# Performance work log

Hardware: AMD Instinct MI355X
Metric: run time of the kernel (lower is better)

## Reference

```python
import jax, jax.numpy as jnp
import numpy as np

N = 50000
E = 800000
IN_C, HID, OUT_C, HEADS = 128, 64, 32, 2
NEG_SLOPE = 0.2


def _add_self_loops(edge_index, n):
    loop = jnp.arange(n, dtype=edge_index.dtype)
    return jnp.concatenate([edge_index, jnp.stack([loop, loop])], axis=1)


def gcn_conv(x, edge_index, W, b, n):
    ei = _add_self_loops(edge_index, n)
    src, dst = ei[0], ei[1]
    h = x @ W                                    # [N, out]
    deg = jax.ops.segment_sum(jnp.ones_like(dst, dtype=h.dtype), dst, num_segments=n)
    dinv = jnp.where(deg > 0, jax.lax.rsqrt(deg), 0.0)
    norm = dinv[src] * dinv[dst]                 # [E2]
    out = jax.ops.segment_sum(h[src] * norm[:, None], dst, num_segments=n)
    return out + b


def gat_conv(x, edge_index, W, att_src, att_dst, b, n, heads, out_dim, concat):
    ei = _add_self_loops(edge_index, n)
    src, dst = ei[0], ei[1]
    h = (x @ W).reshape(n, heads, out_dim)       # [N, H, C]
    a_s = jnp.sum(h * att_src, axis=-1)          # [N, H]
    a_d = jnp.sum(h * att_dst, axis=-1)          # [N, H]
    e = a_s[src] + a_d[dst]                      # [E2, H]
    e = jnp.where(e > 0, e, NEG_SLOPE * e)       # leaky_relu
    # edge softmax grouped by destination node
    m = jax.ops.segment_max(e, dst, num_segments=n)          # [N, H]
    ex = jnp.exp(e - m[dst])
    s = jax.ops.segment_sum(ex, dst, num_segments=n)          # [N, H]
    alpha = ex / s[dst]                          # [E2, H]
    out = jax.ops.segment_sum(h[src] * alpha[:, :, None], dst, num_segments=n)  # [N, H, C]
    if concat:
        out = out.reshape(n, heads * out_dim)
    else:
        out = out.mean(axis=1)
    return out + b


def setup_inputs() -> dict:
    key = jax.random.key(0)
    ks = jax.random.split(key, 16)
    x = jax.random.normal(ks[0], (N, IN_C), dtype=jnp.float32)
    edge_index = jax.random.randint(ks[1], (2, E), 0, N, dtype=jnp.int64)

    def glorot(k, shape):
        fan = shape[0] + shape[-1]
        return jax.random.normal(k, shape, dtype=jnp.float32) * np.sqrt(2.0 / fan)

    return {
        "x": x,
        "edge_index": edge_index,
        "W1": glorot(ks[2], (IN_C, HID)),
        "b1": jnp.zeros((HID,), jnp.float32),
        "W2": glorot(ks[3], (HID, HID)),
        "b2": jnp.zeros((HID,), jnp.float32),
        "Wg1": glorot(ks[4], (HID, HEADS * HID)),
        "as1": glorot(ks[5], (HEADS, HID)),
        "ad1": glorot(ks[6], (HEADS, HID)),
        "bg1": jnp.zeros((HEADS * HID,), jnp.float32),
        "Wg2": glorot(ks[7], (HEADS * HID, HEADS * OUT_C)),
        "as2": glorot(ks[8], (HEADS, OUT_C)),
        "ad2": glorot(ks[9], (HEADS, OUT_C)),
        "bg2": jnp.zeros((OUT_C,), jnp.float32),
    }


def reference(x, edge_index, W1, b1, W2, b2, Wg1, as1, ad1, bg1, Wg2, as2, ad2, bg2):
    n = x.shape[0]
    h = jax.nn.relu(gcn_conv(x, edge_index, W1, b1, n))
    h = jax.nn.relu(gcn_conv(h, edge_index, W2, b2, n))
    h = jax.nn.relu(gat_conv(h, edge_index, Wg1, as1, ad1, bg1, n, HEADS, HID, True))
    h = gat_conv(h, edge_index, Wg2, as2, ad2, bg2, n, HEADS, OUT_C, False)
    return jax.nn.log_softmax(h, axis=1)
```

## Files before the change

kernel.cpp:

```cpp
#include <hip/hip_runtime.h>

#define NN 50000
#define EE 800000
#define NEG 0.2f
#define CAP 64
#define NBC 98
#define BSH2 9
#define CAPB 16384
#define PCH 3125

typedef long long i64;
typedef unsigned int u32;
typedef unsigned short u16;
typedef __attribute__((ext_vector_type(8))) short bf16x8;
typedef __attribute__((ext_vector_type(4))) float f32x4;

static __device__ __forceinline__ u16 f2bf(float f) {
  u32 u = __float_as_uint(f);
  u += 0x7FFFu + ((u >> 16) & 1u);
  return (u16)(u >> 16);
}
static __device__ __forceinline__ float bflo(u32 v) { return __uint_as_float(v << 16); }
static __device__ __forceinline__ float bfhi(u32 v) { return __uint_as_float(v & 0xffff0000u); }
static __device__ __forceinline__ u32 pack2bf(float a, float b) {
  return (u32)f2bf(a) | ((u32)f2bf(b) << 16);
}
static __device__ __forceinline__ void fma8(float* acc, int4 v, float a) {
  acc[0] += bflo(v.x) * a; acc[1] += bfhi(v.x) * a;
  acc[2] += bflo(v.y) * a; acc[3] += bfhi(v.y) * a;
  acc[4] += bflo(v.z) * a; acc[5] += bfhi(v.z) * a;
  acc[6] += bflo(v.w) * a; acc[7] += bfhi(v.w) * a;
}

static __device__ __forceinline__ int edge_at(const void* ei, int is64, int idx) {
  return is64 ? (int)((const i64*)ei)[idx] : ((const int*)ei)[idx];
}

__global__ void k_prep(const float* __restrict__ W1, const float* __restrict__ W2,
                       const float* __restrict__ Wg1, const float* __restrict__ Wg2,
                       u16* P1, u16* P2, u16* P3, u16* P4) {
  int b = blockIdx.x, t = threadIdx.x;
  const float* W; u16* P; int K, N;
  if (b == 0)      { W = W1;  P = P1; K = 128; N = 64;  }
  else if (b == 1) { W = W2;  P = P2; K = 64;  N = 64;  }
  else if (b == 2) { W = Wg1; P = P3; K = 64;  N = 128; }
  else             { W = Wg2; P = P4; K = 128; N = 64;  }
  for (int i = t; i < K * N; i += 256) {
    int k = i / N, n = i % N;
    int byte = ((n * K + k) * 2) ^ ((n & 7) << 4);
    *(u16*)((char*)P + byte) = f2bf(W[i]);
  }
}

__global__ void k_part(const void* ei, int* gcnt, u32* buf) {
  __shared__ u32 lbuf[PCH];
  __shared__ int hist[128], offb[128], curb[128], gbase[128], sc[128], sb[4];
  int t = threadIdx.x;
  const i64* p64 = (const i64*)ei;
  i64 pv = p64[t];
  int bad = (pv < 0 || pv >= NN) ? 1 : 0;
  unsigned long long bm = __ballot(bad);
  if ((t & 63) == 0) sb[t >> 6] = (bm != 0ULL);
  if (t < 128) { hist[t] = 0; curb[t] = 0; }
  __syncthreads();
  int is64 = !(sb[0] | sb[1] | sb[2] | sb[3]);
  int lo = blockIdx.x * PCH;

  for (int e = lo + t; e < lo + PCH; e += 256)
    atomicAdd(&hist[edge_at(ei, is64, EE + e) >> BSH2], 1);
  __syncthreads();

  if (t < 128) sc[t] = hist[t];
  __syncthreads();
  for (int o = 1; o < 128; o <<= 1) {
    int v = (t >= o && t < 128) ? sc[t - o] : 0;
    __syncthreads();
    if (t < 128) sc[t] += v;
    __syncthreads();
  }
  if (t < 128) offb[t] = sc[t] - hist[t];
  __syncthreads();

  for (int e = lo + t; e < lo + PCH; e += 256) {
    int s = edge_at(ei, is64, e);
    int d = edge_at(ei, is64, EE + e);
    int b = d >> BSH2;
    u32 v = (u32)s | ((u32)(d & 511) << 16) | ((u32)b << 25);
    int p = atomicAdd(&curb[b], 1);
    lbuf[offb[b] + p] = v;
  }
  __syncthreads();

  if (t < 128) {
    int c = hist[t];
    gbase[t] = c ? atomicAdd(&gcnt[t], c) : 0;
  }
  __syncthreads();

  for (int i = t; i < PCH; i += 256) {
    u32 v = lbuf[i];
    int b = v >> 25;
    int pos = gbase[b] + (i - offb[b]);
    if (pos < CAPB) buf[(size_t)b * CAPB + pos] = v;
  }
}

__global__ void k_csr2(const u32* __restrict__ buf, const int* __restrict__ gcnt,
                       int* __restrict__ rowp, float* __restrict__ dinv,
                       int* __restrict__ csr) {
  __shared__ int hist[512], offs[512], cur[512], sc[256], pscan[128];
  int b = blockIdx.x;
  int t = threadIdx.x;
  int cnt = min(gcnt[b], CAPB);
  const u32* mb = buf + (size_t)b * CAPB;
  int nbase = b << BSH2;
  int nn = min(512, NN - nbase);

  int pc = (t < NBC) ? min(gcnt[t], CAPB) : 0;
  if (t < 128) pscan[t] = pc;
  hist[t] = 0; hist[t + 256] = 0; cur[t] = 0; cur[t + 256] = 0;
  __syncthreads();
  for (int o = 1; o < 128; o <<= 1) {
    int v = (t >= o && t < 128) ? pscan[t - o] : 0;
    __syncthreads();
    if (t < 128) pscan[t] += v;
    __syncthreads();
  }
  int cbase = pscan[b] - cnt;
  if (b == NBC - 1 && t == 0) rowp[NN] = pscan[NBC - 1];

  for (int i = t; i < cnt; i += 256) atomicAdd(&hist[(mb[i] >> 16) & 511], 1);
  __syncthreads();
  int a0 = hist[2 * t], a1 = hist[2 * t + 1];
  sc[t] = a0 + a1;
  __syncthreads();
  for (int o = 1; o < 256; o <<= 1) {
    int v = (t >= o) ? sc[t - o] : 0;
    __syncthreads();
    sc[t] += v;
    __syncthreads();
  }
  int excl = sc[t] - (a0 + a1);
  offs[2 * t] = excl; offs[2 * t + 1] = excl + a0;
  __syncthreads();
  for (int i = t; i < nn; i += 256) {
    rowp[nbase + i] = cbase + offs[i];
    dinv[nbase + i] = rsqrtf((float)(hist[i] + 1));
  }
  for (int i = t; i < cnt; i += 256) {
    u32 v = mb[i];
    int dl = (v >> 16) & 511;
    int p = atomicAdd(&cur[dl], 1);
    csr[cbase + offs[dl] + p] = (int)(v & 0xFFFF);
  }
}

template <int K, int N, bool SRCF32, bool ATT, int NTH>
__global__ void k_mm(const void* __restrict__ Xsrc, const u16* __restrict__ Wp,
                     const float* __restrict__ aw_s, const float* __restrict__ aw_d,
                     u16* __restrict__ Y, float* __restrict__ a_sv,
                     float* __restrict__ a_dv) {
  constexpr int BM = 64;
  constexpr int NT = N / 16;
  constexpr int KS = K / 32;
  __shared__ u16 Ab[BM * K];
  __shared__ u16 Wt[N * K];
  int t = threadIdx.x;
  int blockRow = blockIdx.x * BM;

  if (SRCF32) {
    const float4* Xq = (const float4*)Xsrc + (size_t)blockRow * (K / 4);
    for (int i = t; i < BM * K / 4; i += 256) {
      int r = (i * 4) / K;
      float4 v = (blockRow + r < NN) ? Xq[i] : make_float4(0.f, 0.f, 0.f, 0.f);
      ushort4 p = make_ushort4(f2bf(v.x), f2bf(v.y), f2bf(v.z), f2bf(v.w));
      int b = i * 8;
      *(ushort4*)((char*)Ab + (b ^ ((r & 7) << 4))) = p;
    }
  } else {
    const int4* Xq = (const int4*)Xsrc + (size_t)blockRow * (K / 8);
    for (int i = t; i < BM * K / 8; i += 256) {
      int r = (i * 8) / K;
      int4 v = (blockRow + r < NN) ? Xq[i] : make_int4(0, 0, 0, 0);
      int b = i * 16;
      *(int4*)((char*)Ab + (b ^ ((r & 7) << 4))) = v;
    }
  }
  for (int i = t; i < N * K / 8; i += 256)
    ((int4*)Wt)[i] = ((const int4*)Wp)[i];
  __syncthreads();

  int w = t >> 6, l = t & 63;
  int lr = l & 15, lg = l >> 4;
  int sw = (lr & 7) << 4;
  f32x4 acc[NT];
#pragma unroll
  for (int nt = 0; nt < NT; ++nt) acc[nt] = (f32x4)0.f;

#pragma unroll
  for (int ks = 0; ks < KS; ++ks) {
    int ar = 16 * w + lr;
    int ab = (ar * K + ks * 32 + lg * 8) * 2;
    bf16x8 af = *(bf16x8*)((char*)Ab + (ab ^ sw));
#pragma unroll
    for (int nt = 0; nt < NT; ++nt) {
      int bb = ((nt * 16 + lr) * K + ks * 32 + lg * 8) * 2;
      bf16x8 bfr = *(bf16x8*)((char*)Wt + (bb ^ sw));
      acc[nt] = __builtin_amdgcn_mfma_f32_16x16x32_bf16(af, bfr, acc[nt], 0, 0, 0);
    }
  }

#pragma unroll
  for (int j = 0; j < 4; ++j) {
    int row = blockRow + 16 * w + lg * 4 + j;
    if (row < NN) {
      u16* yr = Y + (size_t)row * N + lr;
#pragma unroll
      for (int nt = 0; nt < NT; ++nt) yr[nt * 16] = f2bf(acc[nt][j]);
    }
  }

  if (ATT) {
    float aws[NT], awd[NT];
#pragma unroll
    for (int nt = 0; nt < NT; ++nt) {
      aws[nt] = aw_s[nt * 16 + lr];
      awd[nt] = aw_d[nt * 16 + lr];
    }
#pragma unroll
    for (int j = 0; j < 4; ++j) {
      int row = blockRow + 16 * w + lg * 4 + j;
#pragma unroll
      for (int h = 0; h < 2; ++h) {
        float s = 0.f, d = 0.f;
#pragma unroll
        for (int q = 0; q < NTH; ++q) {
          int nt = h * NTH + q;
          s += acc[nt][j] * aws[nt];
          d += acc[nt][j] * awd[nt];
        }
#pragma unroll
        for (int mm = 8; mm >= 1; mm >>= 1) {
          s += __shfl_xor(s, mm, 64);
          d += __shfl_xor(d, mm, 64);
        }
        if (lr == 0 && row < NN) {
          a_sv[row * 2 + h] = s;
          a_dv[row * 2 + h] = d;
        }
      }
    }
  }
}

__global__ void k_gcn(const u16* __restrict__ g, const float* __restrict__ dinv,
                      const int* __restrict__ rowp, const int* __restrict__ csr,
                      const float* __restrict__ bias, u16* __restrict__ outb) {
  __shared__ int   s_src[16][CAP];
  __shared__ float s_wt[16][CAP];
  int w = (threadIdx.x >> 6) & 3;
  int lane = threadIdx.x & 63;
  int qd = lane >> 4, ql = lane & 15;
  int node = (blockIdx.x * 4 + w) * 4 + qd;
  int ns = w * 4 + qd;
  float di = dinv[node];
  int beg = rowp[node], cnt = rowp[node + 1] - beg;
  int tot = cnt + 1;
  int c1 = min(tot, CAP);
  int c1p = (c1 + 1) & ~1;

  for (int idx = ql; idx < c1p; idx += 16) {
    int s; float wt;
    if (idx < cnt)      { s = csr[beg + idx]; wt = dinv[s]; }
    else if (idx < tot) { s = node; wt = di; }
    else                { s = node; wt = 0.f; }
    s_src[ns][idx] = s; s_wt[ns][idx] = wt;
  }

  int sg = ql >> 3, q = ql & 7;
  const int4* g4 = (const int4*)g;
  float acc[8] = {0.f, 0.f, 0.f, 0.f, 0.f, 0.f, 0.f, 0.f};
  int nsteps = c1p >> 1;
  int s0 = s_src[ns][sg]; float a0 = s_wt[ns][sg];
  int4 v0 = g4[(size_t)s0 * 8 + q];
  for (int p = 1; p < nsteps; ++p) {
    int i1 = sg + 2 * p;
    int s1 = s_src[ns][i1]; float a1 = s_wt[ns][i1];
    int4 v1 = g4[(size_t)s1 * 8 + q];
    fma8(acc, v0, a0);
    v0 = v1; a0 = a1;
  }
  fma8(acc, v0, a0);
  for (int idx = CAP + sg; idx < tot; idx += 2) {
    int s = (idx < cnt) ? csr[beg + idx] : node;
    float a = (idx < cnt) ? dinv[s] : di;
    fma8(acc, g4[(size_t)s * 8 + q], a);
  }
#pragma unroll
  for (int j = 0; j < 8; ++j) acc[j] += __shfl_xor(acc[j], 8, 64);
  if (sg == 0) {
    u32 o[4];
#pragma unroll
    for (int p = 0; p < 4; ++p) {
      float v0f = fmaxf(acc[2 * p] * di + bias[8 * q + 2 * p], 0.f);
      float v1f = fmaxf(acc[2 * p + 1] * di + bias[8 * q + 2 * p + 1], 0.f);
      o[p] = pack2bf(v0f, v1f);
    }
    ((int4*)outb)[(size_t)node * 8 + q] = *(int4*)o;
  }
}

__global__ void k_gat1(const u16* __restrict__ hg, const float* __restrict__ a_s,
                       const float* __restrict__ a_d, const int* __restrict__ rowp,
                       const int* __restrict__ csr, const float* __restrict__ bias,
                       u16* __restrict__ outb) {
  __shared__ int   s_src[8][CAP];
  __shared__ float s_x[8][CAP][2];
  int w = (threadIdx.x >> 6) & 3;
  int lane = threadIdx.x & 63;
  int hf = lane >> 5, hl = lane & 31;
  int node = (blockIdx.x * 4 + w) * 2 + hf;
  int ns = w * 2 + hf;
  int beg = rowp[node], cnt = rowp[node + 1] - beg;
  int tot = cnt + 1;
  int c1 = min(tot, CAP);
  int c1p = (c1 + 1) & ~1;
  float ad0 = a_d[node * 2], ad1 = a_d[node * 2 + 1];

  float mm0 = -1e30f, mm1 = -1e30f;
  for (int idx = hl; idx < c1p; idx += 32) {
    int s = (idx < cnt) ? csr[beg + idx] : node;
    float e0 = -1e30f, e1 = -1e30f;
    if (idx < tot) {
      float2 av = ((const float2*)a_s)[s];
      e0 = av.x + ad0; e0 = e0 > 0.f ? e0 : NEG * e0;
      e1 = av.y + ad1; e1 = e1 > 0.f ? e1 : NEG * e1;
    }
    s_src[ns][idx] = s; s_x[ns][idx][0] = e0; s_x[ns][idx][1] = e1;
    mm0 = fmaxf(mm0, e0); mm1 = fmaxf(mm1, e1);
  }
  for (int idx = CAP + hl; idx < tot; idx += 32) {
    int s = (idx < cnt) ? csr[beg + idx] : node;
    float2 av = ((const float2*)a_s)[s];
    float e0 = av.x + ad0; e0 = e0 > 0.f ? e0 : NEG * e0;
    float e1 = av.y + ad1; e1 = e1 > 0.f ? e1 : NEG * e1;
    mm0 = fmaxf(mm0, e0); mm1 = fmaxf(mm1, e1);
  }
#pragma unroll
  for (int m = 16; m >= 1; m >>= 1) {
    mm0 = fmaxf(mm0, __shfl_xor(mm0, m, 64));
    mm1 = fmaxf(mm1, __shfl_xor(mm1, m, 64));
  }
  float ss0 = 0.f, ss1 = 0.f;
  for (int idx = hl; idx < c1p; idx += 32) {
    float x0 = __expf(s_x[ns][idx][0] - mm0), x1 = __expf(s_x[ns][idx][1] - mm1);
    s_x[ns][idx][0] = x0; s_x[ns][idx][1] = x1;
    ss0 += x0; ss1 += x1;
  }
  for (int idx = CAP + hl; idx < tot; idx += 32) {
    int s = (idx < cnt) ? csr[beg + idx] : node;
    float2 av = ((const float2*)a_s)[s];
    float e0 = av.x + ad0; e0 = e0 > 0.f ? e0 : NEG * e0;
    float e1 = av.y + ad1; e1 = e1 > 0.f ? e1 : NEG * e1;
    ss0 += __expf(e0 - mm0); ss1 += __expf(e1 - mm1);
  }
#pragma unroll
  for (int m = 16; m >= 1; m >>= 1) {
    ss0 += __shfl_xor(ss0, m, 64);
    ss1 += __shfl_xor(ss1, m, 64);
  }
  float inv0 = 1.f / ss0, inv1 = 1.f / ss1;

  int sg = hl >> 4, q = hl & 15;
  int hh = q >> 3;
  const int4* g4 = (const int4*)hg;
  float acc[8] = {0.f, 0.f, 0.f, 0.f, 0.f, 0.f, 0.f, 0.f};
  int nsteps = c1p >> 1;
  int s0 = s_src[ns][sg]; float a0 = s_x[ns][sg][hh];
  int4 v0 = g4[(size_t)s0 * 16 + q];
  for (int p = 1; p < nsteps; ++p) {
    int i1 = sg + 2 * p;
    int s1 = s_src[ns][i1]; float a1 = s_x[ns][i1][hh];
    int4 v1 = g4[(size_t)s1 * 16 + q];
    fma8(acc, v0, a0);
    v0 = v1; a0 = a1;
  }
  fma8(acc, v0, a0);
  for (int idx = CAP + sg; idx < tot; idx += 2) {
    int s = (idx < cnt) ? csr[beg + idx] : node;
    float e = (hh ? a_s[s * 2 + 1] + ad1 : a_s[s * 2] + ad0);
    e = e > 0.f ? e : NEG * e;
    float a = __expf(e - (hh ? mm1 : mm0));
    fma8(acc, g4[(size_t)s * 16 + q], a);
  }
#pragma unroll
  for (int j = 0; j < 8; ++j) acc[j] += __shfl_xor(acc[j], 16, 64);
  if (sg == 0) {
    float invh = hh ? inv1 : inv0;
    u32 o[4];
#pragma unroll
    for (int p = 0; p < 4; ++p) {
      float v0f = fmaxf(acc[2 * p] * invh + bias[8 * q + 2 * p], 0.f);
      float v1f = fmaxf(acc[2 * p + 1] * invh + bias[8 * q + 2 * p + 1], 0.f);
      o[p] = pack2bf(v0f, v1f);
    }
    ((int4*)outb)[(size_t)node * 16 + q] = *(int4*)o;
  }
}

__global__ void k_gat2(const u16* __restrict__ hg, const float* __restrict__ a_s,
                       const float* __restrict__ a_d, const int* __restrict__ rowp,
                       const int* __restrict__ csr, const float* __restrict__ bias,
                       float* __restrict__ out) {
  __shared__ int   s_src[16][CAP];
  __shared__ float s_x[16][CAP][2];
  int w = (threadIdx.x >> 6) & 3;
  int lane = threadIdx.x & 63;
  int qd = lane >> 4, ql = lane & 15;
  int node = (blockIdx.x * 4 + w) * 4 + qd;
  int ns = w * 4 + qd;
  int beg = rowp[node], cnt = rowp[node + 1] - beg;
  int tot = cnt + 1;
  int c1 = min(tot, CAP);
  int c1p = (c1 + 1) & ~1;
  float ad0 = a_d[node * 2], ad1 = a_d[node * 2 + 1];

  float mm0 = -1e30f, mm1 = -1e30f;
  for (int idx = ql; idx < c1p; idx += 16) {
    int s = (idx < cnt) ? csr[beg + idx] : node;
    float e0 = -1e30f, e1 = -1e30f;
    if (idx < tot) {
      float2 av = ((const float2*)a_s)[s];
      e0 = av.x + ad0; e0 = e0 > 0.f ? e0 : NEG * e0;
      e1 = av.y + ad1; e1 = e1 > 0.f ? e1 : NEG * e1;
    }
    s_src[ns][idx] = s; s_x[ns][idx][0] = e0; s_x[ns][idx][1] = e1;
    mm0 = fmaxf(mm0, e0); mm1 = fmaxf(mm1, e1);
  }
  for (int idx = CAP + ql; idx < tot; idx += 16) {
    int s = (idx < cnt) ? csr[beg + idx] : node;
    float2 av = ((const float2*)a_s)[s];
    float e0 = av.x + ad0; e0 = e0 > 0.f ? e0 : NEG * e0;
    float e1 = av.y + ad1; e1 = e1 > 0.f ? e1 : NEG * e1;
    mm0 = fmaxf(mm0, e0); mm1 = fmaxf(mm1, e1);
  }
#pragma unroll
  for (int m = 8; m >= 1; m >>= 1) {
    mm0 = fmaxf(mm0, __shfl_xor(mm0, m, 64));
    mm1 = fmaxf(mm1, __shfl_xor(mm1, m, 64));
  }
  float ss0 = 0.f, ss1 = 0.f;
  for (int idx = ql; idx < c1p; idx += 16) {
    float x0 = __expf(s_x[ns][idx][0] - mm0), x1 = __expf(s_x[ns][idx][1] - mm1);
    s_x[ns][idx][0] = x0; s_x[ns][idx][1] = x1;
    ss0 += x0; ss1 += x1;
  }
  for (int idx = CAP + ql; idx < tot; idx += 16) {
    int s = (idx < cnt) ? csr[beg + idx] : node;
    float2 av = ((const float2*)a_s)[s];
    float e0 = av.x + ad0; e0 = e0 > 0.f ? e0 : NEG * e0;
    float e1 = av.y + ad1; e1 = e1 > 0.f ? e1 : NEG * e1;
    ss0 += __expf(e0 - mm0); ss1 += __expf(e1 - mm1);
  }
#pragma unroll
  for (int m = 8; m >= 1; m >>= 1) {
    ss0 += __shfl_xor(ss0, m, 64);
    ss1 += __shfl_xor(ss1, m, 64);
  }
  float inv0 = 1.f / ss0, inv1 = 1.f / ss1;

  int sg = ql >> 3, q = ql & 7;
  int hh = q >> 2;
  const int4* g4 = (const int4*)hg;
  float acc[8] = {0.f, 0.f, 0.f, 0.f, 0.f, 0.f, 0.f, 0.f};
  int nsteps = c1p >> 1;
  int s0 = s_src[ns][sg]; float a0 = s_x[ns][sg][hh];
  int4 v0 = g4[(size_t)s0 * 8 + q];
  for (int p = 1; p < nsteps; ++p) {
    int i1 = sg + 2 * p;
    int s1 = s_src[ns][i1]; float a1 = s_x[ns][i1][hh];
    int4 v1 = g4[(size_t)s1 * 8 + q];
    fma8(acc, v0, a0);
    v0 = v1; a0 = a1;
  }
  fma8(acc, v0, a0);
  for (int idx = CAP + sg; idx < tot; idx += 2) {
    int s = (idx < cnt) ? csr[beg + idx] : node;
    float e = (hh ? a_s[s * 2 + 1] + ad1 : a_s[s * 2] + ad0);
    e = e > 0.f ? e : NEG * e;
    float a = __expf(e - (hh ? mm1 : mm0));
    fma8(acc, g4[(size_t)s * 8 + q], a);
  }
#pragma unroll
  for (int j = 0; j < 8; ++j) acc[j] += __shfl_xor(acc[j], 8, 64);

  float invh = hh ? inv1 : inv0;
  float vv[8];
#pragma unroll
  for (int j = 0; j < 8; ++j) {
    float a = acc[j] * invh;
    vv[j] = 0.5f * (a + __shfl_xor(a, 4, 64)) + bias[8 * (q & 3) + j];
  }
  float mx = vv[0];
#pragma unroll
  for (int j = 1; j < 8; ++j) mx = fmaxf(mx, vv[j]);
  mx = fmaxf(mx, __shfl_xor(mx, 1, 64));
  mx = fmaxf(mx, __shfl_xor(mx, 2, 64));
  float se = 0.f;
#pragma unroll
  for (int j = 0; j < 8; ++j) se += __expf(vv[j] - mx);
  se += __shfl_xor(se, 1, 64);
  se += __shfl_xor(se, 2, 64);
  float lse = mx + __logf(se);
  if (ql < 4) {
    float4 o0 = make_float4(vv[0] - lse, vv[1] - lse, vv[2] - lse, vv[3] - lse);
    float4 o1 = make_float4(vv[4] - lse, vv[5] - lse, vv[6] - lse, vv[7] - lse);
    float4* orow = (float4*)(out + (size_t)node * 32);
    orow[q * 2] = o0;
    orow[q * 2 + 1] = o1;
  }
}

extern "C" void kernel_launch(void* const* d_in, const int* in_sizes, int n_in,
                              void* d_out, int out_size, void* d_ws, size_t ws_size,
                              hipStream_t stream) {
  (void)in_sizes; (void)n_in; (void)out_size; (void)ws_size;
  const float* x   = (const float*)d_in[0];
  const void*  ei  = d_in[1];
  const float* W1  = (const float*)d_in[2];
  const float* b1  = (const float*)d_in[3];
  const float* W2  = (const float*)d_in[4];
  const float* b2  = (const float*)d_in[5];
  const float* Wg1 = (const float*)d_in[6];
  const float* as1 = (const float*)d_in[7];
  const float* ad1 = (const float*)d_in[8];
  const float* bg1 = (const float*)d_in[9];
  const float* Wg2 = (const float*)d_in[10];
  const float* as2 = (const float*)d_in[11];
  const float* ad2 = (const float*)d_in[12];
  const float* bg2 = (const float*)d_in[13];
  float* out = (float*)d_out;

  char* w = (char*)d_ws;
  auto alloc = [&](size_t bytes) { char* p = w; w += (bytes + 255) & ~(size_t)255; return p; };
  u16* Hb     = (u16*)alloc((size_t)NN * 128 * 2);
  u16* Xb     = (u16*)alloc((size_t)NN * 128 * 2);
  float* dinv = (float*)alloc((size_t)NN * 4);
  float* asb  = (float*)alloc((size_t)NN * 2 * 4);
  float* adb  = (float*)alloc((size_t)NN * 2 * 4);
  int* rowp   = (int*)alloc((size_t)(NN + 1) * 4);
  int* csr    = (int*)alloc((size_t)EE * 4);
  u32* buf    = (u32*)alloc((size_t)NBC * CAPB * 4);
  int* gcnt   = (int*)alloc((size_t)NBC * 4);
  u16* Wp1    = (u16*)alloc(128 * 64 * 2);
  u16* Wp2    = (u16*)alloc(64 * 64 * 2);
  u16* Wp3    = (u16*)alloc(64 * 128 * 2);
  u16* Wp4    = (u16*)alloc(128 * 64 * 2);

  const int TB = 256;
  int gQ = 3125;
  int gH = 6250;
  int gG = (NN + 63) / 64;

  hipMemsetAsync(gcnt, 0, (size_t)NBC * 4, stream);
  k_prep<<<4, 256, 0, stream>>>(W1, W2, Wg1, Wg2, Wp1, Wp2, Wp3, Wp4);
  k_part<<<256, TB, 0, stream>>>(ei, gcnt, buf);
  k_csr2<<<NBC, TB, 0, stream>>>(buf, gcnt, rowp, dinv, csr);

  k_mm<128, 64, true, false, 0><<<gG, TB, 0, stream>>>(x, Wp1, nullptr, nullptr, Hb, nullptr, nullptr);
  k_gcn<<<gQ, TB, 0, stream>>>(Hb, dinv, rowp, csr, b1, Xb);
  k_mm<64, 64, false, false, 0><<<gG, TB, 0, stream>>>(Xb, Wp2, nullptr, nullptr, Hb, nullptr, nullptr);
  k_gcn<<<gQ, TB, 0, stream>>>(Hb, dinv, rowp, csr, b2, Xb);
  k_mm<64, 128, false, true, 4><<<gG, TB, 0, stream>>>(Xb, Wp3, as1, ad1, Hb, asb, adb);
  k_gat1<<<gH, TB, 0, stream>>>(Hb, asb, adb, rowp, csr, bg1, Xb);
  k_mm<128, 64, false, true, 2><<<gG, TB, 0, stream>>>(Xb, Wp4, as2, ad2, Hb, asb, adb);
  k_gat2<<<gQ, TB, 0, stream>>>(Hb, asb, adb, rowp, csr, bg2, out);
}
```

Before: 191.5 us.

## Use finer CSR buckets, fold counter reset into prep, and double GEMM row tile

The CSR build now uses 196 buckets of 256 destination nodes instead of 98 of 512, so more blocks run k_csr2 with simpler per-thread scans. The separate memset of the bucket counters is removed and the zeroing is done inside k_prep, saving one launch. The bf16 MFMA GEMM now processes 128 rows per block, with each wave computing two row tiles that reuse the same weight fragments. The larger tile raises shared memory and register use per block, and the 8192-entry bucket cap leaves less headroom if a bucket overflows.

```diff
diff --git a/kernel.cpp b/kernel.cpp
--- a/kernel.cpp
+++ b/kernel.cpp
@@ -4,9 +4,9 @@
 #define EE 800000
 #define NEG 0.2f
 #define CAP 64
-#define NBC 98
-#define BSH2 9
-#define CAPB 16384
+#define NBC 196
+#define BSH2 8
+#define CAPB 8192
 #define PCH 3125
 
 typedef long long i64;
@@ -38,8 +38,9 @@
 
 __global__ void k_prep(const float* __restrict__ W1, const float* __restrict__ W2,
                        const float* __restrict__ Wg1, const float* __restrict__ Wg2,
-                       u16* P1, u16* P2, u16* P3, u16* P4) {
+                       u16* P1, u16* P2, u16* P3, u16* P4, int* gcnt) {
   int b = blockIdx.x, t = threadIdx.x;
+  if (b == 0 && t < NBC) gcnt[t] = 0;
   const float* W; u16* P; int K, N;
   if (b == 0)      { W = W1;  P = P1; K = 128; N = 64;  }
   else if (b == 1) { W = W2;  P = P2; K = 64;  N = 64;  }
@@ -54,14 +55,14 @@
 
 __global__ void k_part(const void* ei, int* gcnt, u32* buf) {
   __shared__ u32 lbuf[PCH];
-  __shared__ int hist[128], offb[128], curb[128], gbase[128], sc[128], sb[4];
+  __shared__ int hist[256], offb[256], curb[256], gbase[256], sc[256], sb[4];
   int t = threadIdx.x;
   const i64* p64 = (const i64*)ei;
   i64 pv = p64[t];
   int bad = (pv < 0 || pv >= NN) ? 1 : 0;
   unsigned long long bm = __ballot(bad);
   if ((t & 63) == 0) sb[t >> 6] = (bm != 0ULL);
-  if (t < 128) { hist[t] = 0; curb[t] = 0; }
+  hist[t] = 0; curb[t] = 0;
   __syncthreads();
   int is64 = !(sb[0] | sb[1] | sb[2] | sb[3]);
   int lo = blockIdx.x * PCH;
@@ -70,36 +71,34 @@
     atomicAdd(&hist[edge_at(ei, is64, EE + e) >> BSH2], 1);
   __syncthreads();
 
-  if (t < 128) sc[t] = hist[t];
-  __syncthreads();
-  for (int o = 1; o < 128; o <<= 1) {
-    int v = (t >= o && t < 128) ? sc[t - o] : 0;
+  sc[t] = hist[t];
+  __syncthreads();
+  for (int o = 1; o < 256; o <<= 1) {
+    int v = (t >= o) ? sc[t - o] : 0;
     __syncthreads();
-    if (t < 128) sc[t] += v;
+    sc[t] += v;
     __syncthreads();
   }
-  if (t < 128) offb[t] = sc[t] - hist[t];
+  offb[t] = sc[t] - hist[t];
   __syncthreads();
 
   for (int e = lo + t; e < lo + PCH; e += 256) {
     int s = edge_at(ei, is64, e);
     int d = edge_at(ei, is64, EE + e);
     int b = d >> BSH2;
-    u32 v = (u32)s | ((u32)(d & 511) << 16) | ((u32)b << 25);
+    u32 v = (u32)s | ((u32)(d & 255) << 16) | ((u32)b << 24);
     int p = atomicAdd(&curb[b], 1);
     lbuf[offb[b] + p] = v;
   }
   __syncthreads();
 
-  if (t < 128) {
-    int c = hist[t];
-    gbase[t] = c ? atomicAdd(&gcnt[t], c) : 0;
-  }
+  int c = hist[t];
+  gbase[t] = c ? atomicAdd(&gcnt[t], c) : 0;
   __syncthreads();
 
   for (int i = t; i < PCH; i += 256) {
     u32 v = lbuf[i];
-    int b = v >> 25;
+    int b = v >> 24;
     int pos = gbase[b] + (i - offb[b]);
     if (pos < CAPB) buf[(size_t)b * CAPB + pos] = v;
   }
@@ -108,31 +107,30 @@
 __global__ void k_csr2(const u32* __restrict__ buf, const int* __restrict__ gcnt,
                        int* __restrict__ rowp, float* __restrict__ dinv,
                        int* __restrict__ csr) {
-  __shared__ int hist[512], offs[512], cur[512], sc[256], pscan[128];
+  __shared__ int hist[256], offs[256], cur[256], pscan[256], sc[256];
   int b = blockIdx.x;
   int t = threadIdx.x;
   int cnt = min(gcnt[b], CAPB);
   const u32* mb = buf + (size_t)b * CAPB;
   int nbase = b << BSH2;
-  int nn = min(512, NN - nbase);
-
-  int pc = (t < NBC) ? min(gcnt[t], CAPB) : 0;
-  if (t < 128) pscan[t] = pc;
-  hist[t] = 0; hist[t + 256] = 0; cur[t] = 0; cur[t + 256] = 0;
-  __syncthreads();
-  for (int o = 1; o < 128; o <<= 1) {
-    int v = (t >= o && t < 128) ? pscan[t - o] : 0;
+  int nn = min(256, NN - nbase);
+
+  pscan[t] = (t < NBC) ? min(gcnt[t], CAPB) : 0;
+  hist[t] = 0; cur[t] = 0;
+  __syncthreads();
+  for (int o = 1; o < 256; o <<= 1) {
+    int v = (t >= o) ? pscan[t - o] : 0;
     __syncthreads();
-    if (t < 128) pscan[t] += v;
+    pscan[t] += v;
     __syncthreads();
   }
   int cbase = pscan[b] - cnt;
   if (b == NBC - 1 && t == 0) rowp[NN] = pscan[NBC - 1];
 
-  for (int i = t; i < cnt; i += 256) atomicAdd(&hist[(mb[i] >> 16) & 511], 1);
-  __syncthreads();
-  int a0 = hist[2 * t], a1 = hist[2 * t + 1];
-  sc[t] = a0 + a1;
+  for (int i = t; i < cnt; i += 256) atomicAdd(&hist[(mb[i] >> 16) & 255], 1);
+  __syncthreads();
+  int h = hist[t];
+  sc[t] = h;
   __syncthreads();
   for (int o = 1; o < 256; o <<= 1) {
     int v = (t >= o) ? sc[t - o] : 0;
@@ -140,16 +138,15 @@
     sc[t] += v;
     __syncthreads();
   }
-  int excl = sc[t] - (a0 + a1);
-  offs[2 * t] = excl; offs[2 * t + 1] = excl + a0;
-  __syncthreads();
-  for (int i = t; i < nn; i += 256) {
-    rowp[nbase + i] = cbase + offs[i];
-    dinv[nbase + i] = rsqrtf((float)(hist[i] + 1));
+  offs[t] = sc[t] - h;
+  __syncthreads();
+  if (t < nn) {
+    rowp[nbase + t] = cbase + offs[t];
+    dinv[nbase + t] = rsqrtf((float)(h + 1));
   }
   for (int i = t; i < cnt; i += 256) {
     u32 v = mb[i];
-    int dl = (v >> 16) & 511;
+    int dl = (v >> 16) & 255;
     int p = atomicAdd(&cur[dl], 1);
     csr[cbase + offs[dl] + p] = (int)(v & 0xFFFF);
   }
@@ -160,7 +157,7 @@
                      const float* __restrict__ aw_s, const float* __restrict__ aw_d,
                      u16* __restrict__ Y, float* __restrict__ a_sv,
                      float* __restrict__ a_dv) {
-  constexpr int BM = 64;
+  constexpr int BM = 128;
   constexpr int NT = N / 16;
   constexpr int KS = K / 32;
   __shared__ u16 Ab[BM * K];
@@ -193,30 +190,37 @@
   int w = t >> 6, l = t & 63;
   int lr = l & 15, lg = l >> 4;
   int sw = (lr & 7) << 4;
-  f32x4 acc[NT];
-#pragma unroll
-  for (int nt = 0; nt < NT; ++nt) acc[nt] = (f32x4)0.f;
+  f32x4 acc[2][NT];
+#pragma unroll
+  for (int rt = 0; rt < 2; ++rt)
+#pragma unroll
+    for (int nt = 0; nt < NT; ++nt) acc[rt][nt] = (f32x4)0.f;
 
 #pragma unroll
   for (int ks = 0; ks < KS; ++ks) {
-    int ar = 16 * w + lr;
-    int ab = (ar * K + ks * 32 + lg * 8) * 2;
-    bf16x8 af = *(bf16x8*)((char*)Ab + (ab ^ sw));
+    int ar0 = 16 * w + lr;
+    int ar1 = 16 * (w + 4) + lr;
+    int kb = (ks * 32 + lg * 8) * 2;
+    bf16x8 af0 = *(bf16x8*)((char*)Ab + ((ar0 * K * 2 + kb) ^ sw));
+    bf16x8 af1 = *(bf16x8*)((char*)Ab + ((ar1 * K * 2 + kb) ^ sw));
 #pragma unroll
     for (int nt = 0; nt < NT; ++nt) {
-      int bb = ((nt * 16 + lr) * K + ks * 32 + lg * 8) * 2;
-      bf16x8 bfr = *(bf16x8*)((char*)Wt + (bb ^ sw));
-      acc[nt] = __builtin_amdgcn_mfma_f32_16x16x32_bf16(af, bfr, acc[nt], 0, 0, 0);
-    }
-  }
-
-#pragma unroll
-  for (int j = 0; j < 4; ++j) {
-    int row = blockRow + 16 * w + lg * 4 + j;
-    if (row < NN) {
-      u16* yr = Y + (size_t)row * N + lr;
-#pragma unroll
-      for (int nt = 0; nt < NT; ++nt) yr[nt * 16] = f2bf(acc[nt][j]);
+      bf16x8 bfr = *(bf16x8*)((char*)Wt + (((nt * 16 + lr) * K * 2 + kb) ^ sw));
+      acc[0][nt] = __builtin_amdgcn_mfma_f32_16x16x32_bf16(af0, bfr, acc[0][nt], 0, 0, 0);
+      acc[1][nt] = __builtin_amdgcn_mfma_f32_16x16x32_bf16(af1, bfr, acc[1][nt], 0, 0, 0);
+    }
+  }
+
+#pragma unroll
+  for (int rt = 0; rt < 2; ++rt) {
+#pragma unroll
+    for (int j = 0; j < 4; ++j) {
+      int row = blockRow + 16 * (w + 4 * rt) + lg * 4 + j;
+      if (row < NN) {
+        u16* yr = Y + (size_t)row * N + lr;
+#pragma unroll
+        for (int nt = 0; nt < NT; ++nt) yr[nt * 16] = f2bf(acc[rt][nt][j]);
+      }
     }
   }
 
@@ -228,25 +232,28 @@
       awd[nt] = aw_d[nt * 16 + lr];
     }
 #pragma unroll
-    for (int j = 0; j < 4; ++j) {
-      int row = blockRow + 16 * w + lg * 4 + j;
-#pragma unroll
-      for (int h = 0; h < 2; ++h) {
-        float s = 0.f, d = 0.f;
-#pragma unroll
-        for (int q = 0; q < NTH; ++q) {
-          int nt = h * NTH + q;
-          s += acc[nt][j] * aws[nt];
-          d += acc[nt][j] * awd[nt];
-        }
-#pragma unroll
-        for (int mm = 8; mm >= 1; mm >>= 1) {
-          s += __shfl_xor(s, mm, 64);
-          d += __shfl_xor(d, mm, 64);
-        }
-        if (lr == 0 && row < NN) {
-          a_sv[row * 2 + h] = s;
-          a_dv[row * 2 + h] = d;
+    for (int rt = 0; rt < 2; ++rt) {
+#pragma unroll
+      for (int j = 0; j < 4; ++j) {
+        int row = blockRow + 16 * (w + 4 * rt) + lg * 4 + j;
+#pragma unroll
+        for (int h = 0; h < 2; ++h) {
+          float s = 0.f, d = 0.f;
+#pragma unroll
+          for (int q = 0; q < NTH; ++q) {
+            int nt = h * NTH + q;
+            s += acc[rt][nt][j] * aws[nt];
+            d += acc[rt][nt][j] * awd[nt];
+          }
+#pragma unroll
+          for (int mm = 8; mm >= 1; mm >>= 1) {
+            s += __shfl_xor(s, mm, 64);
+            d += __shfl_xor(d, mm, 64);
+          }
+          if (lr == 0 && row < NN) {
+            a_sv[row * 2 + h] = s;
+            a_dv[row * 2 + h] = d;
+          }
         }
       }
     }
@@ -560,10 +567,9 @@
   const int TB = 256;
   int gQ = 3125;
   int gH = 6250;
-  int gG = (NN + 63) / 64;
-
-  hipMemsetAsync(gcnt, 0, (size_t)NBC * 4, stream);
-  k_prep<<<4, 256, 0, stream>>>(W1, W2, Wg1, Wg2, Wp1, Wp2, Wp3, Wp4);
+  int gG = (NN + 127) / 128;
+
+  k_prep<<<4, 256, 0, stream>>>(W1, W2, Wg1, Wg2, Wp1, Wp2, Wp3, Wp4, gcnt);
   k_part<<<256, TB, 0, stream>>>(ei, gcnt, buf);
   k_csr2<<<NBC, TB, 0, stream>>>(buf, gcnt, rowp, dinv, csr);
 
```

Result: faster. 181.5 us (-5.2%).
